# Performance work log

Hardware: AMD Instinct MI355X
Metric: run time of the kernel (lower is better)

## Reference

```python
import math
import jax, jax.numpy as jnp
import numpy as np

B, S, D, H = 4, 2048, 768, 12
HD = D // H  # 64


def setup_inputs() -> dict:
    key = jax.random.key(0)
    ks = jax.random.split(key, 10)
    sc = 0.02
    return {
        "hidden_states": jax.random.normal(ks[0], (B, S, D), dtype=jnp.float32),
        "attention_mask": jax.random.randint(ks[1], (1, H, S, S), 0, 2).astype(jnp.bool_),
        "q_w": jax.random.normal(ks[2], (D, D), dtype=jnp.float32) * sc,
        "q_b": jax.random.normal(ks[3], (D,), dtype=jnp.float32) * sc,
        "k_w": jax.random.normal(ks[4], (D, D), dtype=jnp.float32) * sc,
        "k_b": jax.random.normal(ks[5], (D,), dtype=jnp.float32) * sc,
        "v_w": jax.random.normal(ks[6], (D, D), dtype=jnp.float32) * sc,
        "v_b": jax.random.normal(ks[7], (D,), dtype=jnp.float32) * sc,
        "out_w": jax.random.normal(ks[8], (D, D), dtype=jnp.float32) * sc,
        "out_b": jax.random.normal(ks[9], (D,), dtype=jnp.float32) * sc,
    }


def _split_heads(x):
    # [B, S, D] -> [B, H, S, HD]
    b, s, _ = x.shape
    return x.reshape(b, s, H, HD).transpose(0, 2, 1, 3)


def reference(hidden_states, attention_mask, q_w, q_b, k_w, k_b, v_w, v_b, out_w, out_b):
    q = _split_heads(hidden_states @ q_w.T + q_b)
    k = _split_heads(hidden_states @ k_w.T + k_b)
    v = _split_heads(hidden_states @ v_w.T + v_b)
    scores = jnp.einsum("bhqd,bhkd->bhqk", q, k) / math.sqrt(HD)
    # prune_mode, before softmax: masked_fill(~mask, -inf)
    scores = jnp.where(attention_mask, scores, -jnp.inf)
    probs = jax.nn.softmax(scores, axis=-1)  # [B, H, S, S]
    ctx = jnp.einsum("bhqk,bhkd->bhqd", probs, v)
    ctx = ctx.transpose(0, 2, 1, 3).reshape(hidden_states.shape[0], -1, D)
    return ctx @ out_w.T + out_b
```

## Files before the change

### kernel.cpp

```cpp
#include <hip/hip_runtime.h>
#include <hip/hip_bf16.h>

#define B_ 4
#define S_ 2048
#define D_ 768
#define H_ 12
#define HD_ 64

typedef __attribute__((ext_vector_type(8))) short bf16x8;
typedef __attribute__((ext_vector_type(4))) float floatx4;

#define QSCALE 0.18033688011112042f

__device__ __forceinline__ unsigned short f2bf(float x) {
    union { float f; unsigned int u; } v; v.f = x;
    unsigned int r = v.u + 0x7fffu + ((v.u >> 16) & 1u);
    return (unsigned short)(r >> 16);
}

__device__ __forceinline__ unsigned int pk2bf(float a, float b) {
    __hip_bfloat162 h = __float22bfloat162_rn(make_float2(a, b));
    unsigned int u;
    __builtin_memcpy(&u, &h, 4);
    return u;
}

__device__ __forceinline__ void gload_lds16(const void* g, void* l) {
    __builtin_amdgcn_global_load_lds(
        (const __attribute__((address_space(1))) unsigned int*)g,
        (__attribute__((address_space(3))) unsigned int*)l, 16, 0, 0);
}

__device__ __forceinline__ bf16x8 ld_b64x2(const unsigned short* p) {
    union { bf16x8 v; unsigned long long q[2]; } u;
    u.q[0] = *(const unsigned long long*)p;
    u.q[1] = *(const unsigned long long*)(p + 4);
    return u.v;
}

__global__ void cast_f32_bf16(const float* __restrict__ src,
                              unsigned short* __restrict__ dst, int n4) {
    int i = blockIdx.x * 256 + threadIdx.x;
    if (i >= n4) return;
    float4 f = ((const float4*)src)[i];
    ushort4 o;
    o.x = f2bf(f.x); o.y = f2bf(f.y); o.z = f2bf(f.z); o.w = f2bf(f.w);
    ((ushort4*)dst)[i] = o;
}

__global__ void cast_w4(const float* __restrict__ w0, const float* __restrict__ w1,
                        const float* __restrict__ w2, const float* __restrict__ w3,
                        unsigned short* __restrict__ dst, int n4 ) {
    const float* src = (blockIdx.y == 0) ? w0 : (blockIdx.y == 1) ? w1
                     : (blockIdx.y == 2) ? w2 : w3;
    unsigned short* d = dst + (size_t)blockIdx.y * (size_t)n4 * 4;
    int i = blockIdx.x * 256 + threadIdx.x;
    if (i >= n4) return;
    float4 f = ((const float4*)src)[i];
    ushort4 o;
    o.x = f2bf(f.x); o.y = f2bf(f.y); o.z = f2bf(f.z); o.w = f2bf(f.w);
    ((ushort4*)d)[i] = o;
}

__global__ void pack_mask(const int* __restrict__ mask,
                          unsigned long long* __restrict__ bits) {
    size_t gw = (size_t)(blockIdx.x * 256 + threadIdx.x) >> 6;
    int lane = threadIdx.x & 63;
    size_t base = gw * 256;
    unsigned long long b0 = __ballot(mask[base + lane] != 0);
    unsigned long long b1 = __ballot(mask[base + 64 + lane] != 0);
    unsigned long long b2 = __ballot(mask[base + 128 + lane] != 0);
    unsigned long long b3 = __ballot(mask[base + 192 + lane] != 0);
    if (lane == 0) {
        bits[gw * 4 + 0] = b0; bits[gw * 4 + 1] = b1;
        bits[gw * 4 + 2] = b2; bits[gw * 4 + 3] = b3;
    }
}

__global__ __launch_bounds__(256) void qkv_gemm(
    const unsigned short* __restrict__ Xb,
    const unsigned short* __restrict__ Wq, const unsigned short* __restrict__ Wk,
    const unsigned short* __restrict__ Wv,
    const float* __restrict__ bq, const float* __restrict__ bk,
    const float* __restrict__ bv,
    unsigned short* __restrict__ Qo, unsigned short* __restrict__ Ko,
    unsigned short* __restrict__ Vo)
{
    const int z = blockIdx.z;
    const unsigned short* W = (z == 0) ? Wq : (z == 1) ? Wk : Wv;
    const float* bias = (z == 0) ? bq : (z == 1) ? bk : bv;
    unsigned short* Out = (z == 0) ? Qo : (z == 1) ? Ko : Vo;
    const float scale = (z == 0) ? QSCALE : 1.0f;

    const int m0 = blockIdx.x * 128;
    const int n0 = blockIdx.y * 128;

    __shared__ alignas(16) unsigned short SM[8192];
    unsigned short* As = SM;
    unsigned short* Bs = SM + 4096;

    const int t = threadIdx.x;
    const int lane = t & 63, w = t >> 6;
    const int c = lane & 15, quad = lane >> 4;
    const int wm = (w & 1) * 64, wn = (w >> 1) * 64;

    floatx4 acc[4][4];
#pragma unroll
    for (int i = 0; i < 4; i++)
#pragma unroll
        for (int j = 0; j < 4; j++) acc[i][j] = (floatx4){0.f, 0.f, 0.f, 0.f};

    for (int k0 = 0; k0 < 768; k0 += 32) {
#pragma unroll
        for (int i = 0; i < 2; i++) {
            int chunk = i * 4 + w;
            int row = chunk * 16 + (lane >> 2);
            int c8 = (lane & 3) * 8;
            gload_lds16(&Xb[(size_t)(m0 + row) * 768 + k0 + c8], &As[chunk * 512]);
            gload_lds16(&W [(size_t)(n0 + row) * 768 + k0 + c8], &Bs[chunk * 512]);
        }
        __syncthreads();
        bf16x8 a[4], b[4];
#pragma unroll
        for (int i = 0; i < 4; i++)
            a[i] = *(const bf16x8*)&As[(wm + i * 16 + c) * 32 + quad * 8];
#pragma unroll
        for (int j = 0; j < 4; j++)
            b[j] = *(const bf16x8*)&Bs[(wn + j * 16 + c) * 32 + quad * 8];
#pragma unroll
        for (int i = 0; i < 4; i++)
#pragma unroll
            for (int j = 0; j < 4; j++)
                acc[i][j] = __builtin_amdgcn_mfma_f32_16x16x32_bf16(
                    a[i], b[j], acc[i][j], 0, 0, 0);
        __syncthreads();
    }

    const int bb = m0 >> 11, ssb = m0 & 2047;
    if (z == 2) {
#pragma unroll
        for (int half = 0; half < 2; half++) {
            if ((w >> 1) == half) {
#pragma unroll
                for (int j = 0; j < 4; j++) {
                    int n_l = j * 16 + c;
                    float bias_n = bias[n0 + half * 64 + n_l];
#pragma unroll
                    for (int i = 0; i < 4; i++) {
#pragma unroll
                        for (int r = 0; r < 4; r++) {
                            int m = wm + i * 16 + quad * 4 + r;
                            int ms = m ^ (c << 3);
                            SM[n_l * 128 + ms] = f2bf(acc[i][j][r] + bias_n);
                        }
                    }
                }
            }
            __syncthreads();
#pragma unroll
            for (int rb = 0; rb < 2; rb++) {
                int n_l = (t >> 3) + rb * 32;
                int ch = t & 7;
                int n_abs = n0 + half * 64 + n_l;
                int hh = n_abs >> 6, dd = n_abs & 63;
                unsigned short* dst =
                    Out + (((size_t)(bb * H_ + hh)) * 64 + dd) * S_ + ssb;
#pragma unroll
                for (int p = 0; p < 2; p++) {
                    int mc = ch + p * 8;
                    uint4 v = *(const uint4*)&SM[n_l * 128 + ((mc ^ (n_l & 15)) * 8)];
                    *(uint4*)&dst[mc * 8] = v;
                }
            }
            __syncthreads();
        }
    } else {
#pragma unroll
        for (int half = 0; half < 2; half++) {
            if ((w >> 1) == half) {
#pragma unroll
                for (int j = 0; j < 4; j++) {
                    float bias_n = bias[n0 + half * 64 + j * 16 + c];
#pragma unroll
                    for (int i = 0; i < 4; i++) {
#pragma unroll
                        for (int r = 0; r < 4; r++) {
                            int m = wm + i * 16 + quad * 4 + r;
                            int chunk = (j * 2 + (c >> 3)) ^ ((m >> 1) & 7);
                            SM[m * 64 + chunk * 8 + (c & 7)] =
                                f2bf((acc[i][j][r] + bias_n) * scale);
                        }
                    }
                }
            }
            __syncthreads();
            {
                int hh = (n0 >> 6) + half;
                unsigned short* dst =
                    Out + ((size_t)(bb * H_ + hh) * S_ + ssb) * 64;
#pragma unroll
                for (int i = 0; i < 4; i++) {
                    int idx = i * 256 + t;
                    int m = idx >> 3, ch = idx & 7;
                    uint4 v = *(const uint4*)&SM[m * 64 + ((ch ^ ((m >> 1) & 7)) * 8)];
                    *(uint4*)&dst[(size_t)m * 64 + ch * 8] = v;
                }
            }
            __syncthreads();
        }
    }
}

__global__ __launch_bounds__(256) void out_gemm(
    const unsigned short* __restrict__ Cb, const unsigned short* __restrict__ Wo,
    const float* __restrict__ bo, float* __restrict__ out)
{
    const int m0 = blockIdx.x * 128;
    const int n0 = blockIdx.y * 128;

    __shared__ alignas(16) unsigned short SM[8192];
    unsigned short* As = SM;
    unsigned short* Bs = SM + 4096;

    const int t = threadIdx.x;
    const int lane = t & 63, w = t >> 6;
    const int c = lane & 15, quad = lane >> 4;
    const int wm = (w & 1) * 64, wn = (w >> 1) * 64;

    floatx4 acc[4][4];
#pragma unroll
    for (int i = 0; i < 4; i++)
#pragma unroll
        for (int j = 0; j < 4; j++) acc[i][j] = (floatx4){0.f, 0.f, 0.f, 0.f};

    for (int k0 = 0; k0 < 768; k0 += 32) {
#pragma unroll
        for (int i = 0; i < 2; i++) {
            int chunk = i * 4 + w;
            int row = chunk * 16 + (lane >> 2);
            int c8 = (lane & 3) * 8;
            gload_lds16(&Cb[(size_t)(m0 + row) * 768 + k0 + c8], &As[chunk * 512]);
            gload_lds16(&Wo[(size_t)(n0 + row) * 768 + k0 + c8], &Bs[chunk * 512]);
        }
        __syncthreads();
        bf16x8 a[4], b[4];
#pragma unroll
        for (int i = 0; i < 4; i++)
            a[i] = *(const bf16x8*)&As[(wm + i * 16 + c) * 32 + quad * 8];
#pragma unroll
        for (int j = 0; j < 4; j++)
            b[j] = *(const bf16x8*)&Bs[(wn + j * 16 + c) * 32 + quad * 8];
#pragma unroll
        for (int i = 0; i < 4; i++)
#pragma unroll
            for (int j = 0; j < 4; j++)
                acc[i][j] = __builtin_amdgcn_mfma_f32_16x16x32_bf16(
                    a[i], b[j], acc[i][j], 0, 0, 0);
        __syncthreads();
    }

    float* SMf = (float*)SM;
#pragma unroll
    for (int qtr = 0; qtr < 4; qtr++) {
        if ((qtr >> 1) == (wn >> 6)) {
            int j0 = (qtr & 1) * 2;
#pragma unroll
            for (int jj = 0; jj < 2; jj++) {
                int j = j0 + jj;
                float bias_n = bo[n0 + wn + j * 16 + c];
                int chunk = jj * 4 + (c >> 2);
#pragma unroll
                for (int i = 0; i < 4; i++) {
#pragma unroll
                    for (int r = 0; r < 4; r++) {
                        int m = wm + i * 16 + quad * 4 + r;
                        SMf[m * 32 + ((chunk ^ (m & 7)) * 4) + (c & 3)] =
                            acc[i][j][r] + bias_n;
                    }
                }
            }
        }
        __syncthreads();
#pragma unroll
        for (int i = 0; i < 4; i++) {
            int idx = i * 256 + t;
            int m = idx >> 3, ch = idx & 7;
            float4 v = *(const float4*)&SMf[m * 32 + ((ch ^ (m & 7)) * 4)];
            *(float4*)&out[(size_t)(m0 + m) * 768 + n0 + qtr * 32 + ch * 4] = v;
        }
        __syncthreads();
    }
}

__global__ __launch_bounds__(256) void attn(
    const unsigned short* __restrict__ Q, const unsigned short* __restrict__ K,
    const unsigned short* __restrict__ Vt,
    const unsigned long long* __restrict__ mbits,
    unsigned short* __restrict__ ctx)
{
    const int qt = blockIdx.x;
    const int bh = blockIdx.y;
    const int b = bh / H_, h = bh % H_;

    const unsigned short* Qp = Q + (size_t)bh * S_ * 64 + (size_t)qt * 128 * 64;
    const unsigned short* Kp = K + (size_t)bh * S_ * 64;
    const unsigned short* Vp = Vt + (size_t)bh * 64 * S_;

    __shared__ alignas(16) unsigned short Ks[2][64 * 64];
    __shared__ alignas(16) unsigned short Vs[2][64 * 64];
    __shared__ alignas(16) unsigned short Ps[4][16 * 68];

    const int t = threadIdx.x;
    const int lane = t & 63, w = t >> 6;
    const int c = lane & 15, quad = lane >> 4;

    bf16x8 aq[2][2];
#pragma unroll
    for (int st = 0; st < 2; st++) {
        aq[st][0] = *(const bf16x8*)&Qp[(size_t)(w * 32 + st * 16 + c) * 64 + quad * 8];
        aq[st][1] = *(const bf16x8*)&Qp[(size_t)(w * 32 + st * 16 + c) * 64 + 32 + quad * 8];
    }

    const unsigned long long* mrow =
        mbits + ((size_t)h * S_ + qt * 128 + w * 32 + quad * 4) * (S_ / 64);

    floatx4 acc_o[2][4];
#pragma unroll
    for (int st = 0; st < 2; st++)
#pragma unroll
        for (int i = 0; i < 4; i++) acc_o[st][i] = (floatx4){0.f, 0.f, 0.f, 0.f};
    float lp[2][4] = {{0.f, 0.f, 0.f, 0.f}, {0.f, 0.f, 0.f, 0.f}};

    const int srow = (lane >> 3);
    const int rc0 = ((quad     ) ^ (c & 7)) * 8;
    const int rc1 = ((quad + 4) ^ (c & 7)) * 8;

#pragma unroll
    for (int i = 0; i < 2; i++) {
        int chunk = i * 4 + w;
        int row = chunk * 8 + srow;
        int col8 = (((lane & 7) ^ ((row >> 2) & 7))) * 8;
        gload_lds16(&Kp[(size_t)row * 64 + col8], &Ks[0][chunk * 512]);
        gload_lds16(&Vp[(size_t)row * S_ + col8], &Vs[0][chunk * 512]);
    }

    for (int kt = 0; kt < S_ / 64; kt++) {
        const int cur = kt & 1;
        __syncthreads();
        if (kt + 1 < S_ / 64) {
#pragma unroll
            for (int i = 0; i < 2; i++) {
                int chunk = i * 4 + w;
                int row = chunk * 8 + srow;
                int col8 = (((lane & 7) ^ ((row >> 2) & 7))) * 8;
                gload_lds16(&Kp[(size_t)((kt + 1) * 64 + row) * 64 + col8],
                            &Ks[cur ^ 1][chunk * 512]);
                gload_lds16(&Vp[(size_t)row * S_ + (kt + 1) * 64 + col8],
                            &Vs[cur ^ 1][chunk * 512]);
            }
        }

#pragma unroll
        for (int st = 0; st < 2; st++) {
            floatx4 sacc[4];
#pragma unroll
            for (int nt = 0; nt < 4; nt++) {
                int kr = 4 * c + nt;
                bf16x8 bk0 = *(const bf16x8*)&Ks[cur][kr * 64 + rc0];
                bf16x8 bk1 = *(const bf16x8*)&Ks[cur][kr * 64 + rc1];
                floatx4 zz = (floatx4){0.f, 0.f, 0.f, 0.f};
                zz = __builtin_amdgcn_mfma_f32_16x16x32_bf16(aq[st][0], bk0, zz, 0, 0, 0);
                zz = __builtin_amdgcn_mfma_f32_16x16x32_bf16(aq[st][1], bk1, zz, 0, 0, 0);
                sacc[nt] = zz;
            }

            asm volatile("" ::: "memory");
#pragma unroll
            for (int r = 0; r < 4; r++) {
                unsigned int nib =
                    (unsigned int)(mrow[st * 16 * (S_ / 64) + r * (S_ / 64) + kt] >> (4 * c)) & 15u;
                float p0 = (nib & 1u) ? __builtin_amdgcn_exp2f(sacc[0][r]) : 0.f;
                float p1 = (nib & 2u) ? __builtin_amdgcn_exp2f(sacc[1][r]) : 0.f;
                float p2 = (nib & 4u) ? __builtin_amdgcn_exp2f(sacc[2][r]) : 0.f;
                float p3 = (nib & 8u) ? __builtin_amdgcn_exp2f(sacc[3][r]) : 0.f;
                lp[st][r] += (p0 + p1) + (p2 + p3);
                unsigned long long pk =
                    (unsigned long long)pk2bf(p0, p1) |
                    ((unsigned long long)pk2bf(p2, p3) << 32);
                *(unsigned long long*)&Ps[w][(quad * 4 + r) * 68 + 4 * c] = pk;
            }
            asm volatile("" ::: "memory");

            bf16x8 ap0 = ld_b64x2(&Ps[w][c * 68 + quad * 8]);
            bf16x8 ap1 = ld_b64x2(&Ps[w][c * 68 + 32 + quad * 8]);
#pragma unroll
            for (int nt = 0; nt < 4; nt++) {
                int vr = 4 * c + nt;
                bf16x8 bv0 = *(const bf16x8*)&Vs[cur][vr * 64 + rc0];
                bf16x8 bv1 = *(const bf16x8*)&Vs[cur][vr * 64 + rc1];
                acc_o[st][nt] = __builtin_amdgcn_mfma_f32_16x16x32_bf16(ap0, bv0, acc_o[st][nt], 0, 0, 0);
                acc_o[st][nt] = __builtin_amdgcn_mfma_f32_16x16x32_bf16(ap1, bv1, acc_o[st][nt], 0, 0, 0);
            }
        }
    }

#pragma unroll
    for (int st = 0; st < 2; st++)
#pragma unroll
        for (int r = 0; r < 4; r++) {
            float s = lp[st][r];
#pragma unroll
            for (int o = 1; o < 16; o <<= 1) s += __shfl_xor(s, o, 64);
            lp[st][r] = s;
        }

#pragma unroll
    for (int st = 0; st < 2; st++)
#pragma unroll
        for (int nt = 0; nt < 4; nt++)
#pragma unroll
            for (int r = 0; r < 4; r++) {
                int qrow = qt * 128 + w * 32 + st * 16 + quad * 4 + r;
                int dd = 4 * c + nt;
                float v = acc_o[st][nt][r] / lp[st][r];
                ctx[((size_t)b * S_ + qrow) * 768 + h * 64 + dd] = f2bf(v);
            }
}

extern "C" void kernel_launch(void* const* d_in, const int* in_sizes, int n_in,
                              void* d_out, int out_size, void* d_ws, size_t ws_size,
                              hipStream_t stream) {
    const float* hs    = (const float*)d_in[0];
    const int*   mask  = (const int*)d_in[1];
    const float* q_w   = (const float*)d_in[2];
    const float* q_b   = (const float*)d_in[3];
    const float* k_w   = (const float*)d_in[4];
    const float* k_b   = (const float*)d_in[5];
    const float* v_w   = (const float*)d_in[6];
    const float* v_b   = (const float*)d_in[7];
    const float* out_w = (const float*)d_in[8];
    const float* out_b = (const float*)d_in[9];
    float* out = (float*)d_out;

    unsigned short* Xb  = (unsigned short*)d_ws;
    unsigned short* Wqb = Xb + 6291456;
    unsigned short* Wkb = Wqb + 589824;
    unsigned short* Wvb = Wkb + 589824;
    unsigned short* Wob = Wvb + 589824;
    unsigned short* Qb  = Wob + 589824;
    unsigned short* Kb  = Qb + 6291456;
    unsigned short* Vtb = Kb + 6291456;
    unsigned short* Cb  = Vtb + 6291456;
    unsigned long long* mbits = (unsigned long long*)(Cb + 6291456);

    cast_f32_bf16<<<6144, 256, 0, stream>>>(hs, Xb, 1572864);
    cast_w4<<<dim3(576, 4), 256, 0, stream>>>(q_w, k_w, v_w, out_w, Wqb, 147456);
    pack_mask<<<49152, 256, 0, stream>>>(mask, mbits);
    qkv_gemm<<<dim3(64, 6, 3), 256, 0, stream>>>(Xb, Wqb, Wkb, Wvb,
                                                 q_b, k_b, v_b, Qb, Kb, Vtb);
    attn<<<dim3(16, 48), 256, 0, stream>>>(Qb, Kb, Vtb, mbits, Cb);
    out_gemm<<<dim3(64, 6), 256, 0, stream>>>(Cb, Wob, out_b, out);
}
```

Measured before the change: 500.0 us.

## Merge prep kernels, double-buffer GEMM loads, halve out_gemm M tile

Three preprocessing kernels (activation cast, weight cast, mask bit-packing) are merged into one launch to cut launch overhead. Both the QKV and output GEMMs now double-buffer their LDS tiles, issuing the next K-slice's global-to-LDS loads before computing the current one, and they drop one barrier per iteration. The output GEMM M tile is halved to 64 rows, doubling its grid so more CUs are busy. The cost is more LDS per block, which may lower occupancy.

```diff
diff --git a/kernel.cpp b/kernel.cpp
--- a/kernel.cpp
+++ b/kernel.cpp
@@ -38,42 +38,43 @@
     return u.v;
 }
 
-__global__ void cast_f32_bf16(const float* __restrict__ src,
-                              unsigned short* __restrict__ dst, int n4) {
-    int i = blockIdx.x * 256 + threadIdx.x;
-    if (i >= n4) return;
-    float4 f = ((const float4*)src)[i];
-    ushort4 o;
-    o.x = f2bf(f.x); o.y = f2bf(f.y); o.z = f2bf(f.z); o.w = f2bf(f.w);
-    ((ushort4*)dst)[i] = o;
-}
-
-__global__ void cast_w4(const float* __restrict__ w0, const float* __restrict__ w1,
-                        const float* __restrict__ w2, const float* __restrict__ w3,
-                        unsigned short* __restrict__ dst, int n4 ) {
-    const float* src = (blockIdx.y == 0) ? w0 : (blockIdx.y == 1) ? w1
-                     : (blockIdx.y == 2) ? w2 : w3;
-    unsigned short* d = dst + (size_t)blockIdx.y * (size_t)n4 * 4;
-    int i = blockIdx.x * 256 + threadIdx.x;
-    if (i >= n4) return;
-    float4 f = ((const float4*)src)[i];
-    ushort4 o;
-    o.x = f2bf(f.x); o.y = f2bf(f.y); o.z = f2bf(f.z); o.w = f2bf(f.w);
-    ((ushort4*)d)[i] = o;
-}
-
-__global__ void pack_mask(const int* __restrict__ mask,
-                          unsigned long long* __restrict__ bits) {
-    size_t gw = (size_t)(blockIdx.x * 256 + threadIdx.x) >> 6;
-    int lane = threadIdx.x & 63;
-    size_t base = gw * 256;
-    unsigned long long b0 = __ballot(mask[base + lane] != 0);
-    unsigned long long b1 = __ballot(mask[base + 64 + lane] != 0);
-    unsigned long long b2 = __ballot(mask[base + 128 + lane] != 0);
-    unsigned long long b3 = __ballot(mask[base + 192 + lane] != 0);
-    if (lane == 0) {
-        bits[gw * 4 + 0] = b0; bits[gw * 4 + 1] = b1;
-        bits[gw * 4 + 2] = b2; bits[gw * 4 + 3] = b3;
+__global__ void prep(const float* __restrict__ hs,
+                     const float* __restrict__ w0, const float* __restrict__ w1,
+                     const float* __restrict__ w2, const float* __restrict__ w3,
+                     const int* __restrict__ mask,
+                     unsigned short* __restrict__ Xb,
+                     unsigned short* __restrict__ Wb,
+                     unsigned long long* __restrict__ bits) {
+    int bid = blockIdx.x;
+    int t = threadIdx.x;
+    if (bid < 6144) {
+        int i = bid * 256 + t;
+        float4 f = ((const float4*)hs)[i];
+        ushort4 o;
+        o.x = f2bf(f.x); o.y = f2bf(f.y); o.z = f2bf(f.z); o.w = f2bf(f.w);
+        ((ushort4*)Xb)[i] = o;
+    } else if (bid < 8448) {
+        int q = bid - 6144;
+        int wid = q / 576;
+        const float* src = (wid == 0) ? w0 : (wid == 1) ? w1 : (wid == 2) ? w2 : w3;
+        unsigned short* d = Wb + (size_t)wid * 589824;
+        int i = (q - wid * 576) * 256 + t;
+        float4 f = ((const float4*)src)[i];
+        ushort4 o;
+        o.x = f2bf(f.x); o.y = f2bf(f.y); o.z = f2bf(f.z); o.w = f2bf(f.w);
+        ((ushort4*)d)[i] = o;
+    } else {
+        size_t gw = ((size_t)(bid - 8448) * 256 + t) >> 6;
+        int lane = t & 63;
+        size_t base = gw * 256;
+        unsigned long long b0 = __ballot(mask[base + lane] != 0);
+        unsigned long long b1 = __ballot(mask[base + 64 + lane] != 0);
+        unsigned long long b2 = __ballot(mask[base + 128 + lane] != 0);
+        unsigned long long b3 = __ballot(mask[base + 192 + lane] != 0);
+        if (lane == 0) {
+            bits[gw * 4 + 0] = b0; bits[gw * 4 + 1] = b1;
+            bits[gw * 4 + 2] = b2; bits[gw * 4 + 3] = b3;
+        }
     }
 }
 
@@ -95,31 +96,47 @@
     const int m0 = blockIdx.x * 128;
     const int n0 = blockIdx.y * 128;
 
-    __shared__ alignas(16) unsigned short SM[8192];
-    unsigned short* As = SM;
-    unsigned short* Bs = SM + 4096;
+    __shared__ alignas(16) unsigned short SMall[16384];
+    unsigned short* SM = SMall;
 
     const int t = threadIdx.x;
     const int lane = t & 63, w = t >> 6;
     const int c = lane & 15, quad = lane >> 4;
     const int wm = (w & 1) * 64, wn = (w >> 1) * 64;
 
+    const int srowq = lane >> 2, sc8 = (lane & 3) * 8;
+
     floatx4 acc[4][4];
 #pragma unroll
     for (int i = 0; i < 4; i++)
 #pragma unroll
         for (int j = 0; j < 4; j++) acc[i][j] = (floatx4){0.f, 0.f, 0.f, 0.f};
 
-    for (int k0 = 0; k0 < 768; k0 += 32) {
-#pragma unroll
-        for (int i = 0; i < 2; i++) {
-            int chunk = i * 4 + w;
-            int row = chunk * 16 + (lane >> 2);
-            int c8 = (lane & 3) * 8;
-            gload_lds16(&Xb[(size_t)(m0 + row) * 768 + k0 + c8], &As[chunk * 512]);
-            gload_lds16(&W [(size_t)(n0 + row) * 768 + k0 + c8], &Bs[chunk * 512]);
-        }
+#pragma unroll
+    for (int i = 0; i < 2; i++) {
+        int chunk = i * 4 + w;
+        int row = chunk * 16 + srowq;
+        gload_lds16(&Xb[(size_t)(m0 + row) * 768 + sc8], &SMall[chunk * 512]);
+        gload_lds16(&W [(size_t)(n0 + row) * 768 + sc8], &SMall[4096 + chunk * 512]);
+    }
+
+    for (int it = 0; it < 24; it++) {
+        const int cur = it & 1;
         __syncthreads();
+        if (it + 1 < 24) {
+            int k1 = (it + 1) * 32;
+#pragma unroll
+            for (int i = 0; i < 2; i++) {
+                int chunk = i * 4 + w;
+                int row = chunk * 16 + srowq;
+                gload_lds16(&Xb[(size_t)(m0 + row) * 768 + k1 + sc8],
+                            &SMall[(cur ^ 1) * 8192 + chunk * 512]);
+                gload_lds16(&W [(size_t)(n0 + row) * 768 + k1 + sc8],
+                            &SMall[(cur ^ 1) * 8192 + 4096 + chunk * 512]);
+            }
+        }
+        const unsigned short* As = &SMall[cur * 8192];
+        const unsigned short* Bs = As + 4096;
         bf16x8 a[4], b[4];
 #pragma unroll
         for (int i = 0; i < 4; i++)
@@ -133,8 +150,8 @@
             for (int j = 0; j < 4; j++)
                 acc[i][j] = __builtin_amdgcn_mfma_f32_16x16x32_bf16(
                     a[i], b[j], acc[i][j], 0, 0, 0);
-        __syncthreads();
-    }
+    }
+    __syncthreads();
 
     const int bb = m0 >> 11, ssb = m0 & 2047;
     if (z == 2) {
@@ -215,62 +232,77 @@
     const unsigned short* __restrict__ Cb, const unsigned short* __restrict__ Wo,
     const float* __restrict__ bo, float* __restrict__ out)
 {
-    const int m0 = blockIdx.x * 128;
+    const int m0 = blockIdx.x * 64;
     const int n0 = blockIdx.y * 128;
 
-    __shared__ alignas(16) unsigned short SM[8192];
-    unsigned short* As = SM;
-    unsigned short* Bs = SM + 4096;
+    __shared__ alignas(16) unsigned short SMall[12288];
 
     const int t = threadIdx.x;
     const int lane = t & 63, w = t >> 6;
     const int c = lane & 15, quad = lane >> 4;
-    const int wm = (w & 1) * 64, wn = (w >> 1) * 64;
-
-    floatx4 acc[4][4];
-#pragma unroll
-    for (int i = 0; i < 4; i++)
+    const int wm = (w & 1) * 32, wn = (w >> 1) * 64;
+
+    const int arow = w * 16 + (lane >> 2);
+    const int brow0 = (lane >> 2);
+    const int sc8 = (lane & 3) * 8;
+
+    floatx4 acc[2][4];
+#pragma unroll
+    for (int i = 0; i < 2; i++)
 #pragma unroll
         for (int j = 0; j < 4; j++) acc[i][j] = (floatx4){0.f, 0.f, 0.f, 0.f};
 
-    for (int k0 = 0; k0 < 768; k0 += 32) {
-#pragma unroll
-        for (int i = 0; i < 2; i++) {
-            int chunk = i * 4 + w;
-            int row = chunk * 16 + (lane >> 2);
-            int c8 = (lane & 3) * 8;
-            gload_lds16(&Cb[(size_t)(m0 + row) * 768 + k0 + c8], &As[chunk * 512]);
-            gload_lds16(&Wo[(size_t)(n0 + row) * 768 + k0 + c8], &Bs[chunk * 512]);
-        }
+    gload_lds16(&Cb[(size_t)(m0 + arow) * 768 + sc8], &SMall[w * 512]);
+#pragma unroll
+    for (int i = 0; i < 2; i++) {
+        int chunk = i * 4 + w;
+        gload_lds16(&Wo[(size_t)(n0 + chunk * 16 + brow0) * 768 + sc8],
+                    &SMall[2048 + chunk * 512]);
+    }
+
+    for (int it = 0; it < 24; it++) {
+        const int cur = it & 1;
         __syncthreads();
-        bf16x8 a[4], b[4];
-#pragma unroll
-        for (int i = 0; i < 4; i++)
+        if (it + 1 < 24) {
+            int k1 = (it + 1) * 32;
+            gload_lds16(&Cb[(size_t)(m0 + arow) * 768 + k1 + sc8],
+                        &SMall[(cur ^ 1) * 6144 + w * 512]);
+#pragma unroll
+            for (int i = 0; i < 2; i++) {
+                int chunk = i * 4 + w;
+                gload_lds16(&Wo[(size_t)(n0 + chunk * 16 + brow0) * 768 + k1 + sc8],
+                            &SMall[(cur ^ 1) * 6144 + 2048 + chunk * 512]);
+            }
+        }
+        const unsigned short* As = &SMall[cur * 6144];
+        const unsigned short* Bs = As + 2048;
+        bf16x8 a[2], b[4];
+#pragma unroll
+        for (int i = 0; i < 2; i++)
             a[i] = *(const bf16x8*)&As[(wm + i * 16 + c) * 32 + quad * 8];
 #pragma unroll
         for (int j = 0; j < 4; j++)
             b[j] = *(const bf16x8*)&Bs[(wn + j * 16 + c) * 32 + quad * 8];
 #pragma unroll
-        for (int i = 0; i < 4; i++)
+        for (int i = 0; i < 2; i++)
 #pragma unroll
             for (int j = 0; j < 4; j++)
                 acc[i][j] = __builtin_amdgcn_mfma_f32_16x16x32_bf16(
                     a[i], b[j], acc[i][j], 0, 0, 0);
-        __syncthreads();
-    }
-
-    float* SMf = (float*)SM;
+    }
+    __syncthreads();
+
+    float* SMf = (float*)SMall;
 #pragma unroll
     for (int qtr = 0; qtr < 4; qtr++) {
-        if ((qtr >> 1) == (wn >> 6)) {
-            int j0 = (qtr & 1) * 2;
+        if ((w >> 1) == (qtr >> 1)) {
 #pragma unroll
             for (int jj = 0; jj < 2; jj++) {
-                int j = j0 + jj;
+                int j = (qtr & 1) * 2 + jj;
                 float bias_n = bo[n0 + wn + j * 16 + c];
                 int chunk = jj * 4 + (c >> 2);
 #pragma unroll
-                for (int i = 0; i < 4; i++) {
+                for (int i = 0; i < 2; i++) {
 #pragma unroll
                     for (int r = 0; r < 4; r++) {
                         int m = wm + i * 16 + quad * 4 + r;
@@ -282,7 +314,7 @@
         }
         __syncthreads();
 #pragma unroll
-        for (int i = 0; i < 4; i++) {
+        for (int i = 0; i < 2; i++) {
             int idx = i * 256 + t;
             int m = idx >> 3, ch = idx & 7;
             float4 v = *(const float4*)&SMf[m * 32 + ((ch ^ (m & 7)) * 4)];
@@ -453,11 +485,9 @@
     unsigned short* Cb  = Vtb + 6291456;
     unsigned long long* mbits = (unsigned long long*)(Cb + 6291456);
 
-    cast_f32_bf16<<<6144, 256, 0, stream>>>(hs, Xb, 1572864);
-    cast_w4<<<dim3(576, 4), 256, 0, stream>>>(q_w, k_w, v_w, out_w, Wqb, 147456);
-    pack_mask<<<49152, 256, 0, stream>>>(mask, mbits);
+    prep<<<57600, 256, 0, stream>>>(hs, q_w, k_w, v_w, out_w, mask, Xb, Wqb, mbits);
     qkv_gemm<<<dim3(64, 6, 3), 256, 0, stream>>>(Xb, Wqb, Wkb, Wvb,
                                                  q_b, k_b, v_b, Qb, Kb, Vtb);
     attn<<<dim3(16, 48), 256, 0, stream>>>(Qb, Kb, Vtb, mbits, Cb);
-    out_gemm<<<dim3(64, 6), 256, 0, stream>>>(Cb, Wob, out_b, out);
-}
+    out_gemm<<<dim3(128, 6), 256, 0, stream>>>(Cb, Wob, out_b, out);
+}
```

After: 484.5 us. -3.1%, faster.
